# Optimization experiments

Hardware: AMD Instinct MI355X
Metric: run time of the kernel (lower is better)

The kernel has to match this reference:

```python
import jax, jax.numpy as jnp
import numpy as np

B, S, DIM, H, D = 2, 2048, 1024, 16, 64  # inner_dim = H*D = 1024


def setup_inputs() -> dict:
    key = jax.random.key(0)
    ks = jax.random.split(key, 6)
    hidden_states = jax.random.normal(ks[0], (B, S, DIM), dtype=jnp.float32)
    # proper RoPE angle tables for head_dim=D (interleaved-pair convention)
    inv_freq = 1.0 / (10000.0 ** (np.arange(0, D, 2, dtype=np.float32) / D))  # [D/2]
    ang = np.arange(S, dtype=np.float32)[:, None] * inv_freq[None, :]          # [S, D/2]
    ang = np.repeat(ang, 2, axis=-1)                                           # [S, D] interleaved pairs
    cos = jnp.broadcast_to(jnp.asarray(np.cos(ang)), (B, S, D)).astype(jnp.float32)
    sin = jnp.broadcast_to(jnp.asarray(np.sin(ang)), (B, S, D)).astype(jnp.float32)
    scale = 0.02
    qkv_w = jax.random.normal(ks[1], (3 * H * D, DIM), dtype=jnp.float32) * scale
    qkv_b = jax.random.normal(ks[2], (3 * H * D,), dtype=jnp.float32) * scale
    out_w = jax.random.normal(ks[3], (DIM, H * D), dtype=jnp.float32) * scale
    out_b = jax.random.normal(ks[4], (DIM,), dtype=jnp.float32) * scale
    return {"hidden_states": hidden_states, "cos": cos, "sin": sin,
            "qkv_w": qkv_w, "qkv_b": qkv_b, "out_w": out_w, "out_b": out_b}


def _rotate_half_codec(x):
    # interleaved-pair rotation: (x1, x2) -> (-x2, x1) on consecutive pairs
    xr = x.reshape(*x.shape[:-1], -1, 2)
    x1, x2 = xr[..., 0], xr[..., 1]
    return jnp.stack((-x2, x1), axis=-1).reshape(*x.shape)


def reference(hidden_states, cos, sin, qkv_w, qkv_b, out_w, out_b):
    b = hidden_states.shape[0]
    # fused QKV projection: [B,S,DIM] @ [DIM,3*H*D] + bias
    qkv = jnp.einsum('bsd,ed->bse', hidden_states, qkv_w) + qkv_b
    inner = H * D
    q, k, v = qkv[..., :inner], qkv[..., inner:2 * inner], qkv[..., 2 * inner:]
    # [B,S,H*D] -> [B,H,S,D]
    q = q.reshape(b, -1, H, D).transpose(0, 2, 1, 3)
    k = k.reshape(b, -1, H, D).transpose(0, 2, 1, 3)
    v = v.reshape(b, -1, H, D).transpose(0, 2, 1, 3)
    # partial RoPE: applied only to head 0 (query[:, :1], key[:, :1])
    c = cos[:, None]  # [B,1,S,D]
    s = sin[:, None]
    q0 = q[:, :1] * c + _rotate_half_codec(q[:, :1]) * s
    k0 = k[:, :1] * c + _rotate_half_codec(k[:, :1]) * s
    q = jnp.concatenate([q0, q[:, 1:]], axis=1)
    k = jnp.concatenate([k0, k[:, 1:]], axis=1)
    # non-causal SDPA
    scores = jnp.einsum('bhqd,bhkd->bhqk', q, k) / jnp.sqrt(jnp.asarray(D, q.dtype))
    attn = jax.nn.softmax(scores, axis=-1)
    out = jnp.einsum('bhqk,bhkd->bhqd', attn, v)
    out = out.transpose(0, 2, 1, 3).reshape(b, -1, H * D)  # [B,S,H*D]
    # output projection (dropout is identity in eval)
    return jnp.einsum('bse,de->bsd', out, out_w) + out_b
```

## Files before the change

### kernel.cpp

```cpp
#include <hip/hip_runtime.h>
#include <cstdint>

typedef __bf16 bf16x8 __attribute__((ext_vector_type(8)));
typedef float f32x4 __attribute__((ext_vector_type(4)));
typedef float f32x16 __attribute__((ext_vector_type(16)));
typedef unsigned short u16x8 __attribute__((ext_vector_type(8)));
typedef unsigned short u16x4 __attribute__((ext_vector_type(4)));
typedef unsigned int uint32x4 __attribute__((ext_vector_type(4)));
typedef unsigned int uint_g __attribute__((address_space(1)));
typedef unsigned int uint_l __attribute__((address_space(3)));

#define MFMA16(a, b, c) __builtin_amdgcn_mfma_f32_16x16x32_bf16(a, b, c, 0, 0, 0)
#define MFMA32(a, b, c) __builtin_amdgcn_mfma_f32_32x32x16_bf16(a, b, c, 0, 0, 0)

static __device__ __forceinline__ unsigned short f2bf(float f) {
    unsigned u = __builtin_bit_cast(unsigned, f);
    u += 0x7FFFu + ((u >> 16) & 1u);
    return (unsigned short)(u >> 16);
}
static __device__ __forceinline__ float bf2f(unsigned short h) {
    unsigned u = ((unsigned)h) << 16;
    return __builtin_bit_cast(float, u);
}
static __device__ __forceinline__ void gload16(const unsigned short* g, unsigned short* lds) {
    __builtin_amdgcn_global_load_lds((uint_g*)g, (uint_l*)lds, 16, 0, 0);
}
static __device__ __forceinline__ unsigned cvt_pk_bf16(float a, float b) {
    unsigned r;
    asm("v_cvt_pk_bf16_f32 %0, %1, %2" : "=v"(r) : "v"(a), "v"(b));
    return r;
}

#define SB 2048
#define NROWS 4096
#define DIMM 1024
#define NH 16
#define HD 64

__global__ __launch_bounds__(256) void k_convert(const float* __restrict__ s0,
                                                 const float* __restrict__ s1,
                                                 const float* __restrict__ s2,
                                                 unsigned short* __restrict__ dst) {
    int base = blockIdx.x * 256 + threadIdx.x;
#pragma unroll
    for (int v = 0; v < 4; ++v) {
        int i = base + v * 262144;
        const float* src;
        int rel;
        if (i < 524288) { src = s0; rel = i; }
        else if (i < 917504) { src = s1; rel = i - 524288; }
        else { src = s2; rel = i - 917504; }
        const float4* p = (const float4*)src + (size_t)rel * 2;
        float4 a = p[0], bq = p[1];
        u16x8 o;
        o[0] = f2bf(a.x);  o[1] = f2bf(a.y);  o[2] = f2bf(a.z);  o[3] = f2bf(a.w);
        o[4] = f2bf(bq.x); o[5] = f2bf(bq.y); o[6] = f2bf(bq.z); o[7] = f2bf(bq.w);
        *((u16x8*)dst + i) = o;
    }
}

__global__ void k_rope(unsigned short* __restrict__ qk, const float* __restrict__ cosp,
                       const float* __restrict__ sinp) {
    int row = blockIdx.x;
    int t = threadIdx.x;
    int which = t >> 5;
    int i = t & 31;
    unsigned short* base = qk + (size_t)row * 2048 + which * 1024;
    float x0 = bf2f(base[2 * i]);
    float x1 = bf2f(base[2 * i + 1]);
    float c = cosp[(size_t)row * 64 + 2 * i];
    float sn = sinp[(size_t)row * 64 + 2 * i];
    base[2 * i]     = f2bf(x0 * c - x1 * sn);
    base[2 * i + 1] = f2bf(x1 * c + x0 * sn);
}

template <int MODE, int BM>
__global__ __launch_bounds__(256) void k_gemm_nt(
    const unsigned short* __restrict__ A, const unsigned short* __restrict__ B,
    const float* __restrict__ bias, unsigned short* __restrict__ outQK,
    unsigned short* __restrict__ outVg, float* __restrict__ outF, int M, int N, int K) {
    constexpr int MI = BM / 32;
    __shared__ __align__(16) unsigned short As[BM * 64];
    __shared__ __align__(16) unsigned short Bs[128 * 64];
    const int tid = threadIdx.x;
    const int w = tid >> 6, l = tid & 63, lr = l & 15, lg = l >> 4;
    const int wm = w >> 1, wn = w & 1;
    const int m0 = blockIdx.y * BM, n0 = blockIdx.x * 128;

    f32x4 acc[MI][4];
    f32x4 zero4 = {0.f, 0.f, 0.f, 0.f};
#pragma unroll
    for (int i = 0; i < MI; ++i)
#pragma unroll
        for (int j = 0; j < 4; ++j) acc[i][j] = zero4;

    const int trow = tid >> 3;
    const int tkb = (tid & 7) ^ ((tid >> 3) & 7);
    const unsigned short* Ag = A + (size_t)(m0 + trow) * K + tkb * 8;
    const unsigned short* Bg = B + (size_t)(n0 + trow) * K + tkb * 8;
    const int rsw = (lr & 7) << 3;

    for (int kt = 0; kt < K; kt += 64) {
#pragma unroll
        for (int i = 0; i < BM / 32; ++i)
            gload16(Ag + (size_t)i * 32 * K + kt, (unsigned short*)((char*)As + i * 4096 + w * 1024));
#pragma unroll
        for (int i = 0; i < 4; ++i)
            gload16(Bg + (size_t)i * 32 * K + kt, (unsigned short*)((char*)Bs + i * 4096 + w * 1024));
        asm volatile("s_waitcnt vmcnt(0)" ::: "memory");
        __syncthreads();
        bf16x8 af[MI][2], bfr[4][2];
#pragma unroll
        for (int mi = 0; mi < MI; ++mi)
#pragma unroll
            for (int s = 0; s < 2; ++s)
                af[mi][s] = *(const bf16x8*)&As[(wm * (BM / 2) + mi * 16 + lr) * 64 +
                                                ((s * 32 + lg * 8) ^ rsw)];
#pragma unroll
        for (int ni = 0; ni < 4; ++ni)
#pragma unroll
            for (int s = 0; s < 2; ++s)
                bfr[ni][s] = *(const bf16x8*)&Bs[(wn * 64 + ni * 16 + lr) * 64 +
                                                 ((s * 32 + lg * 8) ^ rsw)];
#pragma unroll
        for (int mi = 0; mi < MI; ++mi)
#pragma unroll
            for (int ni = 0; ni < 4; ++ni)
#pragma unroll
                for (int s = 0; s < 2; ++s)
                    acc[mi][ni] = MFMA16(af[mi][s], bfr[ni][s], acc[mi][ni]);
        __syncthreads();
    }

#pragma unroll
    for (int mi = 0; mi < MI; ++mi)
#pragma unroll
        for (int ni = 0; ni < 4; ++ni) {
            int gc = n0 + wn * 64 + ni * 16 + lr;
            int gr0 = m0 + wm * (BM / 2) + mi * 16 + lg * 4;
            float bv = bias[gc];
            f32x4 v = acc[mi][ni];
            if (MODE == 0) {
                if (gc < 2048) {
#pragma unroll
                    for (int r = 0; r < 4; ++r)
                        outQK[(size_t)(gr0 + r) * 2048 + gc] = f2bf(v[r] + bv);
                } else {
                    int e = gc - 2048;
                    int hh = e >> 6, d = e & 63;
                    int bb = gr0 >> 11, s = gr0 & 2047;
                    int bh = bb * NH + hh;
                    int T = s >> 6, w64 = s & 63;
                    int ks = w64 >> 4, hi8 = (w64 >> 3) & 1, j0 = w64 & 7;
                    int db = d >> 5, lqv = d & 31;
                    u16x4 pk;
#pragma unroll
                    for (int r = 0; r < 4; ++r) pk[r] = f2bf(v[r] + bv);
                    size_t off = ((size_t)((bh * 32 + T) * 8 + db * 4 + ks)) * 512 +
                                 (hi8 * 32 + lqv) * 8 + j0;
                    *(u16x4*)&outVg[off] = pk;
                }
            } else {
#pragma unroll
                for (int r = 0; r < 4; ++r)
                    outF[(size_t)(gr0 + r) * N + gc] = v[r] + bv;
            }
        }
}

#define ATTN_BODY(T, PA, VA0, VA1, PB, VB0, VB1, DOSTAGE)                                \
  {                                                                                      \
    if (DOSTAGE) stageK((T) & 1, (T) + 2);                                               \
    const unsigned short* vtbN = vgb + (size_t)((T) + 1) * 4096;                         \
    _Pragma("unroll") for (int ks = 0; ks < 4; ++ks)                                     \
        VB0[ks] = *(const bf16x8*)&vtbN[(size_t)ks * 512 + l * 8];                       \
    _Pragma("unroll") for (int ks = 0; ks < 4; ++ks)                                     \
        VB1[ks] = *(const bf16x8*)&vtbN[(size_t)(4 + ks) * 512 + l * 8];                 \
    const char* Kb = (const char*)Ks[((T) + 1) & 1];                                     \
    f32x16 s0, s1;                                                                       \
    __builtin_amdgcn_s_setprio(1);                                                       \
    _Pragma("unroll") for (int ds = 0; ds < 4; ++ds) {                                   \
        bf16x8 kf0 = *(const bf16x8*)(Kb + lq * 128 + ((ds * 32 + hi * 16) ^ swz));      \
        bf16x8 kf1 = *(const bf16x8*)(Kb + (32 + lq) * 128 + ((ds * 32 + hi * 16) ^ swz)); \
        s0 = (ds == 0) ? MFMA32(kf0, qf[0], z16) : MFMA32(kf0, qf[ds], s0);              \
        s1 = (ds == 0) ? MFMA32(kf1, qf[0], z16) : MFMA32(kf1, qf[ds], s1);              \
    }                                                                                    \
    _Pragma("unroll") for (int ks = 0; ks < 4; ++ks) {                                   \
        oacc[0] = MFMA32(PA[ks], VA0[ks], oacc[0]);                                      \
        oacc[1] = MFMA32(PA[ks], VA1[ks], oacc[1]);                                      \
        lacc    = MFMA32(PA[ks], vones,   lacc);                                         \
    }                                                                                    \
    __builtin_amdgcn_s_setprio(0);                                                       \
    _Pragma("unroll") for (int r = 0; r < 16; ++r) {                                     \
        s0[r] = __builtin_amdgcn_exp2f(s0[r]);                                           \
        s1[r] = __builtin_amdgcn_exp2f(s1[r]);                                           \
    }                                                                                    \
    _Pragma("unroll") for (int ks = 0; ks < 4; ++ks) {                                   \
        const int k2 = ks & 1;                                                           \
        f32x16& sb = (ks < 2) ? s0 : s1;                                                 \
        unsigned XA = cvt_pk_bf16(sb[8 * k2 + 0], sb[8 * k2 + 1]);                       \
        unsigned YA = cvt_pk_bf16(sb[8 * k2 + 2], sb[8 * k2 + 3]);                       \
        unsigned XB = cvt_pk_bf16(sb[8 * k2 + 4], sb[8 * k2 + 5]);                       \
        unsigned YB = cvt_pk_bf16(sb[8 * k2 + 6], sb[8 * k2 + 7]);                       \
        asm("v_permlane32_swap_b32 %0, %1" : "+v"(XA), "+v"(XB));                        \
        asm("v_permlane32_swap_b32 %0, %1" : "+v"(YA), "+v"(YB));                        \
        uint32x4 pw;                                                                     \
        pw[0] = XA; pw[1] = YA; pw[2] = XB; pw[3] = YB;                                  \
        PB[ks] = __builtin_bit_cast(bf16x8, pw);                                         \
    }                                                                                    \
    if (DOSTAGE) {                                                                      \
        asm volatile("s_waitcnt vmcnt(8)" ::: "memory");                                 \
        __builtin_amdgcn_s_barrier();                                                    \
    }                                                                                    \
  }

__global__ __launch_bounds__(128, 2) void k_attn(const unsigned short* __restrict__ qk,
                                                 const unsigned short* __restrict__ vg,
                                                 unsigned short* __restrict__ ao) {
    const int raw = blockIdx.x;
    const int bid = (raw & 7) * 128 + (raw >> 3);
    const int qt = bid & 31, bh = bid >> 5, b = bh >> 4, h = bh & 15;
    const int tid = threadIdx.x, w = tid >> 6, l = tid & 63;
    const int lq = l & 31, hi = l >> 5;

    __shared__ __align__(16) unsigned short Ks[2][4096];

    const size_t rowbase = (size_t)b * SB;
    const float QSC = 0.18033688011112043f;
    const int qrow = qt * 64 + w * 32 + lq;

    bf16x8 qf[4];
#pragma unroll
    for (int ds = 0; ds < 4; ++ds) {
        u16x8 rawq = *(const u16x8*)&qk[(rowbase + qrow) * 2048 + h * 64 + ds * 16 + hi * 8];
        u16x8 sc;
#pragma unroll
        for (int j = 0; j < 8; ++j) sc[j] = f2bf(bf2f(rawq[j]) * QSC);
        qf[ds] = __builtin_bit_cast(bf16x8, sc);
    }

    u16x8 onesu;
#pragma unroll
    for (int j = 0; j < 8; ++j) onesu[j] = 0x3F80;
    const bf16x8 vones = __builtin_bit_cast(bf16x8, onesu);

    const char* ksrc[4];
#pragma unroll
    for (int j = 0; j < 4; ++j) {
        int Lb = (j * 2 + w) * 1024 + l * 16;
        int r = Lb >> 7, c = Lb & 127;
        int cs = c ^ ((r & 7) << 4);
        ksrc[j] = (const char*)qk + ((size_t)(rowbase + r) * 2048 + 1024 + h * 64) * 2 + cs;
    }
    auto stageK = [&](int bufi, int tg) {
#pragma unroll
        for (int j = 0; j < 4; ++j)
            gload16((const unsigned short*)(ksrc[j] + (size_t)tg * 262144),
                    Ks[bufi] + (j * 2 + w) * 512);
    };

    const unsigned short* vgb = vg + (size_t)bh * 131072;

    f32x16 z16 = {0.f, 0.f, 0.f, 0.f, 0.f, 0.f, 0.f, 0.f,
                  0.f, 0.f, 0.f, 0.f, 0.f, 0.f, 0.f, 0.f};
    f32x16 oacc[2];
    oacc[0] = z16;
    oacc[1] = z16;
    f32x16 lacc = z16;
    const int swz = (l & 7) << 4;

    bf16x8 vfA0[4], vfA1[4], vfB0[4], vfB1[4];
    bf16x8 paA[4], paB[4];

    stageK(0, 0);
    __syncthreads();
    stageK(1, 1);
#pragma unroll
    for (int ks = 0; ks < 4; ++ks)
        vfA0[ks] = *(const bf16x8*)&vgb[(size_t)ks * 512 + l * 8];
#pragma unroll
    for (int ks = 0; ks < 4; ++ks)
        vfA1[ks] = *(const bf16x8*)&vgb[(size_t)(4 + ks) * 512 + l * 8];
    {
        const char* Kb = (const char*)Ks[0];
        f32x16 s0, s1;
#pragma unroll
        for (int ds = 0; ds < 4; ++ds) {
            bf16x8 kf0 = *(const bf16x8*)(Kb + lq * 128 + ((ds * 32 + hi * 16) ^ swz));
            bf16x8 kf1 = *(const bf16x8*)(Kb + (32 + lq) * 128 + ((ds * 32 + hi * 16) ^ swz));
            s0 = (ds == 0) ? MFMA32(kf0, qf[0], z16) : MFMA32(kf0, qf[ds], s0);
            s1 = (ds == 0) ? MFMA32(kf1, qf[0], z16) : MFMA32(kf1, qf[ds], s1);
        }
#pragma unroll
        for (int r = 0; r < 16; ++r) {
            s0[r] = __builtin_amdgcn_exp2f(s0[r]);
            s1[r] = __builtin_amdgcn_exp2f(s1[r]);
        }
#pragma unroll
        for (int ks = 0; ks < 4; ++ks) {
            const int k2 = ks & 1;
            f32x16& sb = (ks < 2) ? s0 : s1;
            unsigned XA = cvt_pk_bf16(sb[8 * k2 + 0], sb[8 * k2 + 1]);
            unsigned YA = cvt_pk_bf16(sb[8 * k2 + 2], sb[8 * k2 + 3]);
            unsigned XB = cvt_pk_bf16(sb[8 * k2 + 4], sb[8 * k2 + 5]);
            unsigned YB = cvt_pk_bf16(sb[8 * k2 + 6], sb[8 * k2 + 7]);
            asm("v_permlane32_swap_b32 %0, %1" : "+v"(XA), "+v"(XB));
            asm("v_permlane32_swap_b32 %0, %1" : "+v"(YA), "+v"(YB));
            uint32x4 pw;
            pw[0] = XA; pw[1] = YA; pw[2] = XB; pw[3] = YB;
            paA[ks] = __builtin_bit_cast(bf16x8, pw);
        }
    }
    asm volatile("s_waitcnt vmcnt(8)" ::: "memory");
    __builtin_amdgcn_s_barrier();

    for (int tt = 0; tt < 15; ++tt) {
        const int t = 2 * tt;
        ATTN_BODY(t,     paA, vfA0, vfA1, paB, vfB0, vfB1, true)
        ATTN_BODY(t + 1, paB, vfB0, vfB1, paA, vfA0, vfA1, true)
    }
    ATTN_BODY(30, paA, vfA0, vfA1, paB, vfB0, vfB1, false)
    __builtin_amdgcn_s_setprio(1);
#pragma unroll
    for (int ks = 0; ks < 4; ++ks) {
        oacc[0] = MFMA32(paB[ks], vfB0[ks], oacc[0]);
        oacc[1] = MFMA32(paB[ks], vfB1[ks], oacc[1]);
        lacc    = MFMA32(paB[ks], vones,   lacc);
    }
    __builtin_amdgcn_s_setprio(0);

#pragma unroll
    for (int r = 0; r < 16; ++r) {
        float inv = __builtin_amdgcn_rcpf(lacc[r]);
        int qv = (r & 3) + 8 * (r >> 2) + 4 * hi;
        int qg = qt * 64 + w * 32 + qv;
        ao[(rowbase + qg) * DIMM + h * 64 + lq] = f2bf(oacc[0][r] * inv);
        ao[(rowbase + qg) * DIMM + h * 64 + 32 + lq] = f2bf(oacc[1][r] * inv);
    }
}

extern "C" void kernel_launch(void* const* d_in, const int* in_sizes, int n_in,
                              void* d_out, int out_size, void* d_ws, size_t ws_size,
                              hipStream_t stream) {
    const float* hidden = (const float*)d_in[0];
    const float* cosp   = (const float*)d_in[1];
    const float* sinp   = (const float*)d_in[2];
    const float* qkv_w  = (const float*)d_in[3];
    const float* qkv_b  = (const float*)d_in[4];
    const float* out_w  = (const float*)d_in[5];
    const float* out_b  = (const float*)d_in[6];
    float* out = (float*)d_out;

    unsigned short* hbf   = (unsigned short*)d_ws;
    unsigned short* wqkv  = hbf + (size_t)NROWS * DIMM;
    unsigned short* wout  = wqkv + (size_t)3072 * DIMM;
    unsigned short* qkbuf = wout + (size_t)DIMM * DIMM;
    unsigned short* vgbuf = qkbuf + (size_t)NROWS * 2048;
    unsigned short* aobuf = hbf;

    k_convert<<<1024, 256, 0, stream>>>(hidden, qkv_w, out_w, hbf);
    k_gemm_nt<0, 128><<<dim3(24, 32), 256, 0, stream>>>(hbf, wqkv, qkv_b, qkbuf, vgbuf,
                                                        nullptr, NROWS, 3072, DIMM);
    k_rope<<<NROWS, 64, 0, stream>>>(qkbuf, cosp, sinp);
    k_attn<<<1024, 128, 0, stream>>>(qkbuf, vgbuf, aobuf);
    k_gemm_nt<1, 64><<<dim3(8, 64), 256, 0, stream>>>(aobuf, wout, out_b, nullptr, nullptr,
                                                      out, NROWS, DIMM, DIMM);
}
```

Measured before the change: 116.7 us.

## Split attention key range across two wave pairs and merge partial sums in LDS

The attention block grows from 2 to 4 waves. Each pair of waves handles half of the 32 key tiles with its own double-buffered K staging, and the second pair's partial O and row-sum accumulators are added into the first pair's through LDS before normalisation and store. The aim is more waves in flight per CU and a shorter serial key loop per wave, so latency is hidden better. The cost is a reduction step with two block barriers, doubled LDS for K, and more register pressure under the new launch bounds. No max subtraction is needed because the original already skips it.

```diff
diff --git a/kernel.cpp b/kernel.cpp
--- a/kernel.cpp
+++ b/kernel.cpp
@@ -170,13 +170,13 @@
 
 #define ATTN_BODY(T, PA, VA0, VA1, PB, VB0, VB1, DOSTAGE)                                \
   {                                                                                      \
-    if (DOSTAGE) stageK((T) & 1, (T) + 2);                                               \
-    const unsigned short* vtbN = vgb + (size_t)((T) + 1) * 4096;                         \
+    if (DOSTAGE) stageK((T) & 1, TB + (T) + 2);                                          \
+    const unsigned short* vtbN = vgb + (size_t)(TB + (T) + 1) * 4096;                    \
     _Pragma("unroll") for (int ks = 0; ks < 4; ++ks)                                     \
         VB0[ks] = *(const bf16x8*)&vtbN[(size_t)ks * 512 + l * 8];                       \
     _Pragma("unroll") for (int ks = 0; ks < 4; ++ks)                                     \
         VB1[ks] = *(const bf16x8*)&vtbN[(size_t)(4 + ks) * 512 + l * 8];                 \
-    const char* Kb = (const char*)Ks[((T) + 1) & 1];                                     \
+    const char* Kb = (const char*)Ks[p][((T) + 1) & 1];                                  \
     f32x16 s0, s1;                                                                       \
     __builtin_amdgcn_s_setprio(1);                                                       \
     _Pragma("unroll") for (int ds = 0; ds < 4; ++ds) {                                   \
@@ -214,20 +214,22 @@
     }                                                                                    \
   }
 
-__global__ __launch_bounds__(128, 2) void k_attn(const unsigned short* __restrict__ qk,
+__global__ __launch_bounds__(256, 4) void k_attn(const unsigned short* __restrict__ qk,
                                                  const unsigned short* __restrict__ vg,
                                                  unsigned short* __restrict__ ao) {
     const int raw = blockIdx.x;
     const int bid = (raw & 7) * 128 + (raw >> 3);
     const int qt = bid & 31, bh = bid >> 5, b = bh >> 4, h = bh & 15;
     const int tid = threadIdx.x, w = tid >> 6, l = tid & 63;
+    const int p = w >> 1, wp = w & 1;
     const int lq = l & 31, hi = l >> 5;
-
-    __shared__ __align__(16) unsigned short Ks[2][4096];
+    const int TB = p * 16;
+
+    __shared__ __align__(16) unsigned short Ks[2][2][4096];
 
     const size_t rowbase = (size_t)b * SB;
     const float QSC = 0.18033688011112043f;
-    const int qrow = qt * 64 + w * 32 + lq;
+    const int qrow = qt * 64 + wp * 32 + lq;
 
     bf16x8 qf[4];
 #pragma unroll
@@ -247,7 +249,7 @@
     const char* ksrc[4];
 #pragma unroll
     for (int j = 0; j < 4; ++j) {
-        int Lb = (j * 2 + w) * 1024 + l * 16;
+        int Lb = (j * 2 + wp) * 1024 + l * 16;
         int r = Lb >> 7, c = Lb & 127;
         int cs = c ^ ((r & 7) << 4);
         ksrc[j] = (const char*)qk + ((size_t)(rowbase + r) * 2048 + 1024 + h * 64) * 2 + cs;
@@ -256,7 +258,7 @@
 #pragma unroll
         for (int j = 0; j < 4; ++j)
             gload16((const unsigned short*)(ksrc[j] + (size_t)tg * 262144),
-                    Ks[bufi] + (j * 2 + w) * 512);
+                    Ks[p][bufi] + (j * 2 + wp) * 512);
     };
 
     const unsigned short* vgb = vg + (size_t)bh * 131072;
@@ -272,17 +274,17 @@
     bf16x8 vfA0[4], vfA1[4], vfB0[4], vfB1[4];
     bf16x8 paA[4], paB[4];
 
-    stageK(0, 0);
+    stageK(0, TB);
     __syncthreads();
-    stageK(1, 1);
+    stageK(1, TB + 1);
 #pragma unroll
     for (int ks = 0; ks < 4; ++ks)
-        vfA0[ks] = *(const bf16x8*)&vgb[(size_t)ks * 512 + l * 8];
+        vfA0[ks] = *(const bf16x8*)&vgb[(size_t)TB * 4096 + (size_t)ks * 512 + l * 8];
 #pragma unroll
     for (int ks = 0; ks < 4; ++ks)
-        vfA1[ks] = *(const bf16x8*)&vgb[(size_t)(4 + ks) * 512 + l * 8];
+        vfA1[ks] = *(const bf16x8*)&vgb[(size_t)TB * 4096 + (size_t)(4 + ks) * 512 + l * 8];
     {
-        const char* Kb = (const char*)Ks[0];
+        const char* Kb = (const char*)Ks[p][0];
         f32x16 s0, s1;
 #pragma unroll
         for (int ds = 0; ds < 4; ++ds) {
@@ -314,12 +316,12 @@
     asm volatile("s_waitcnt vmcnt(8)" ::: "memory");
     __builtin_amdgcn_s_barrier();
 
-    for (int tt = 0; tt < 15; ++tt) {
+    for (int tt = 0; tt < 7; ++tt) {
         const int t = 2 * tt;
         ATTN_BODY(t,     paA, vfA0, vfA1, paB, vfB0, vfB1, true)
         ATTN_BODY(t + 1, paB, vfB0, vfB1, paA, vfA0, vfA1, true)
     }
-    ATTN_BODY(30, paA, vfA0, vfA1, paB, vfB0, vfB1, false)
+    ATTN_BODY(14, paA, vfA0, vfA1, paB, vfB0, vfB1, false)
     __builtin_amdgcn_s_setprio(1);
 #pragma unroll
     for (int ks = 0; ks < 4; ++ks) {
@@ -329,13 +331,30 @@
     }
     __builtin_amdgcn_s_setprio(0);
 
-#pragma unroll
-    for (int r = 0; r < 16; ++r) {
-        float inv = __builtin_amdgcn_rcpf(lacc[r]);
-        int qv = (r & 3) + 8 * (r >> 2) + 4 * hi;
-        int qg = qt * 64 + w * 32 + qv;
-        ao[(rowbase + qg) * DIMM + h * 64 + lq] = f2bf(oacc[0][r] * inv);
-        ao[(rowbase + qg) * DIMM + h * 64 + 32 + lq] = f2bf(oacc[1][r] * inv);
+    float* cb = (float*)&Ks[0][0][0];
+    float* slot = cb + (wp * 64 + l) * 49;
+    __syncthreads();
+    if (p == 1) {
+#pragma unroll
+        for (int r = 0; r < 16; ++r) {
+            slot[r] = oacc[0][r];
+            slot[16 + r] = oacc[1][r];
+            slot[32 + r] = lacc[r];
+        }
+    }
+    __syncthreads();
+    if (p == 0) {
+#pragma unroll
+        for (int r = 0; r < 16; ++r) {
+            float o0 = oacc[0][r] + slot[r];
+            float o1 = oacc[1][r] + slot[16 + r];
+            float lv = lacc[r] + slot[32 + r];
+            float inv = __builtin_amdgcn_rcpf(lv);
+            int qv = (r & 3) + 8 * (r >> 2) + 4 * hi;
+            int qg = qt * 64 + wp * 32 + qv;
+            ao[(rowbase + qg) * DIMM + h * 64 + lq] = f2bf(o0 * inv);
+            ao[(rowbase + qg) * DIMM + h * 64 + 32 + lq] = f2bf(o1 * inv);
+        }
     }
 }
 
@@ -362,7 +381,7 @@
     k_gemm_nt<0, 128><<<dim3(24, 32), 256, 0, stream>>>(hbf, wqkv, qkv_b, qkbuf, vgbuf,
                                                         nullptr, NROWS, 3072, DIMM);
     k_rope<<<NROWS, 64, 0, stream>>>(qkbuf, cosp, sinp);
-    k_attn<<<1024, 128, 0, stream>>>(qkbuf, vgbuf, aobuf);
+    k_attn<<<1024, 256, 0, stream>>>(qkbuf, vgbuf, aobuf);
     k_gemm_nt<1, 64><<<dim3(8, 64), 256, 0, stream>>>(aobuf, wout, out_b, nullptr, nullptr,
                                                       out, NROWS, DIMM, DIMM);
 }
```

Result: slower. 345.9 us (+196.4%).
